# Kernel optimization log

Measured on AMD Instinct MI355X. Metric: run time of the kernel, lower is better.

## Reference

```python
import jax, jax.numpy as jnp
import numpy as np

D = 1024      # hidden_dim
V = 8         # op_vocab_size / num_ops
L = 4         # prog_len
CD = 8        # concept_dim_total (6 + 2)
I = D + CD    # op/program-generator input dim
B, T = 8, 512


def gru(x, h0, W_ih, W_hh, b_ih, b_hh):
    """PyTorch-convention GRU. x: (B,T,In), h0: (B,H). Gate order r,z,n."""
    def step(h, xt):
        gx = xt @ W_ih.T + b_ih            # (B, 3H)
        gh = h @ W_hh.T + b_hh             # (B, 3H)
        xr, xz, xn = jnp.split(gx, 3, axis=-1)
        hr, hz, hn = jnp.split(gh, 3, axis=-1)
        r = jax.nn.sigmoid(xr + hr)
        z = jax.nn.sigmoid(xz + hz)
        n = jnp.tanh(xn + r * hn)
        h_new = (1.0 - z) * n + z * h
        return h_new, h_new
    _, ys = jax.lax.scan(step, h0, jnp.swapaxes(x, 0, 1))
    return jnp.swapaxes(ys, 0, 1)          # (B,T,H)


def _l2norm(x, axis=-1):
    n = jnp.sqrt(jnp.sum(x * x, axis=axis, keepdims=True))
    return x / jnp.maximum(n, 1e-12)


def setup_inputs() -> dict:
    key = jax.random.key(0)
    ks = jax.random.split(key, 24)
    s = 0.02
    inp = {
        "x": jax.random.normal(ks[0], (B, T, D), dtype=jnp.float32),
        "attention_mask": jnp.ones((B, T), dtype=jnp.float32),
        # TemporalEncoder GRU
        "enc_Wih": s * jax.random.normal(ks[1], (3 * D, D), dtype=jnp.float32),
        "enc_Whh": s * jax.random.normal(ks[2], (3 * D, D), dtype=jnp.float32),
        "enc_bih": jnp.zeros((3 * D,), dtype=jnp.float32),
        "enc_bhh": jnp.zeros((3 * D,), dtype=jnp.float32),
        # ConceptClassifier heads (token_type=6, polarity=2)
        "tt_W": s * jax.random.normal(ks[3], (6, D), dtype=jnp.float32),
        "tt_b": jnp.zeros((6,), dtype=jnp.float32),
        "pol_W": s * jax.random.normal(ks[4], (2, D), dtype=jnp.float32),
        "pol_b": jnp.zeros((2,), dtype=jnp.float32),
        # ProgramGenerator
        "c2h_W": s * jax.random.normal(ks[5], (D, I), dtype=jnp.float32),
        "c2h_b": jnp.zeros((D,), dtype=jnp.float32),
        "pg_Wih": s * jax.random.normal(ks[6], (3 * D, I), dtype=jnp.float32),
        "pg_Whh": s * jax.random.normal(ks[7], (3 * D, D), dtype=jnp.float32),
        "pg_bih": jnp.zeros((3 * D,), dtype=jnp.float32),
        "pg_bhh": jnp.zeros((3 * D,), dtype=jnp.float32),
        "proj_W": s * jax.random.normal(ks[8], (V, D), dtype=jnp.float32),
        "proj_b": jnp.zeros((V,), dtype=jnp.float32),
        # NeuralOpLibrary: V ops, each Linear(I,D)-GELU-Linear(D,D)
        "op_W1": s * jax.random.normal(ks[9], (V, D, I), dtype=jnp.float32),
        "op_b1": jnp.zeros((V, D), dtype=jnp.float32),
        "op_W2": s * jax.random.normal(ks[10], (V, D, D), dtype=jnp.float32),
        "op_b2": jnp.zeros((V, D), dtype=jnp.float32),
        # output projection (2D -> D)
        "out_W": s * jax.random.normal(ks[11], (D, 2 * D), dtype=jnp.float32),
        "out_b": jnp.zeros((D,), dtype=jnp.float32),
    }
    return inp


def reference(x, attention_mask, enc_Wih, enc_Whh, enc_bih, enc_bhh,
              tt_W, tt_b, pol_W, pol_b, c2h_W, c2h_b,
              pg_Wih, pg_Whh, pg_bih, pg_bhh, proj_W, proj_b,
              op_W1, op_b1, op_W2, op_b2, out_W, out_b):
    Bx = x.shape[0]
    x = x * attention_mask[..., None]
    # TemporalEncoder: GRU + residual
    h0 = jnp.zeros((Bx, D), dtype=x.dtype)
    x = gru(x, h0, enc_Wih, enc_Whh, enc_bih, enc_bhh) + x        # (B,T,D)

    # concepts
    tt = x @ tt_W.T + tt_b                                        # (B,T,6)
    pol = x @ pol_W.T + pol_b                                     # (B,T,2)
    concept_summary = jnp.concatenate([tt.mean(1), pol.mean(1)], axis=-1)  # (B,8)
    pooled = x.mean(1)                                            # (B,D)
    context = jnp.concatenate([pooled, concept_summary], axis=-1) # (B,I)

    # ProgramGenerator: GRU over zero inputs, h0 from context
    pg_h0 = context @ c2h_W.T + c2h_b                             # (B,D)
    rnn_in = jnp.zeros((Bx, L, I), dtype=x.dtype)
    rnn_out = gru(rnn_in, pg_h0, pg_Wih, pg_Whh, pg_bih, pg_bhh)  # (B,L,D)
    program_logits = rnn_out @ proj_W.T + proj_b                  # (B,L,V)

    # NeuralOpLibrary. The torch code expands token feats to (B,L,T,D) and runs
    # each op redundantly per L; since op outputs are independent of L, the
    # softmax-weighted sum + mean over L equals weighting by the L-averaged
    # softmax weights (identical math).
    token_feats = jnp.concatenate([x, tt, pol], axis=-1)          # (B,T,I)
    h1 = jax.nn.gelu(jnp.einsum('bti,vdi->btvd', token_feats, op_W1) + op_b1,
                     approximate=False)                           # (B,T,V,D)
    op_out = jnp.einsum('btvh,vdh->btvd', h1, op_W2) + op_b2      # (B,T,V,D)
    w = jax.nn.softmax(program_logits, axis=-1).mean(axis=1)      # (B,V)
    out = jnp.einsum('btvd,bv->btd', op_out, w)                   # (B,T,D)

    max_pooled = out.max(axis=1)
    mean_pooled = out.mean(axis=1)
    pooled2 = jnp.concatenate([max_pooled, mean_pooled], axis=-1) # (B,2D)
    z = pooled2 @ out_W.T + out_b                                 # (B,D)

    plf = program_logits.reshape(Bx, -1)                          # (B,L*V)
    pooled_norm = _l2norm(pooled2)
    sim = pooled_norm @ pooled_norm.T                             # (B,B)
    sq = jnp.sum(plf * plf, axis=-1)
    d2 = jnp.maximum(sq[:, None] + sq[None, :] - 2.0 * (plf @ plf.T), 0.0)
    dist = jnp.where(d2 > 0, jnp.sqrt(jnp.where(d2 > 0, d2, 1.0)), 0.0)
    reuse_loss = (sim * dist).mean()

    prog_norm = _l2norm(plf)
    prog_sim = prog_norm @ prog_norm.T
    pos_mask = (sim > 0.7).astype(x.dtype)
    neg_mask = (sim < 0.7).astype(x.dtype)
    pos_loss = (1.0 - prog_sim) * pos_mask
    neg_loss = jax.nn.relu(prog_sim - 0.5) * neg_mask
    contrastive_loss = (pos_loss.sum() + neg_loss.sum()) / (pos_mask.sum() + neg_mask.sum() + 1e-6)
    return (z, reuse_loss, contrastive_loss)
```

## Files before the change

kernel.cpp:

```cpp
#include <hip/hip_runtime.h>
#include <stdint.h>

#define D_   1024
#define T_   512
#define B_   8
#define V_   8
#define I_   1032
#define KP_  1088
#define TDK  3072

typedef __attribute__((ext_vector_type(8))) short bf16x8;
typedef __attribute__((ext_vector_type(4))) float f32x4;

__device__ __forceinline__ ushort f2bf(float f){
  union{ unsigned u; float f; } c; c.f = f;
  unsigned u = c.u;
  return (ushort)((u + 0x7FFFu + ((u>>16)&1u)) >> 16);
}
__device__ __forceinline__ float bf2f(ushort h){
  union{ unsigned u; float f; } c; c.u = ((unsigned)h) << 16; return c.f;
}
__device__ __forceinline__ float sigmoidf_(float x){ return 1.f/(1.f+__expf(-x)); }

#define WAITV(N) do{ asm volatile("s_waitcnt vmcnt(" #N ")" ::: "memory"); __builtin_amdgcn_sched_barrier(0); }while(0)

__device__ __forceinline__ void gload_lds16(const void* g, void* l){
  __builtin_amdgcn_global_load_lds((const __attribute__((address_space(1))) void*)g,
                                   (__attribute__((address_space(3))) void*)l, 16, 0, 0);
}

__global__ __launch_bounds__(256) void k_prep(const float* __restrict__ x, const float* __restrict__ mask,
                                              float* __restrict__ xm, ushort* __restrict__ xmb){
  int i = blockIdx.x*256 + threadIdx.x;
  float4 v = ((const float4*)x)[i];
  float mk = mask[i >> 8];
  v.x*=mk; v.y*=mk; v.z*=mk; v.w*=mk;
  ((float4*)xm)[i] = v;
  ushort4 h; h.x=f2bf(v.x); h.y=f2bf(v.y); h.z=f2bf(v.z); h.w=f2bf(v.w);
  ((ushort4*)xmb)[i] = h;
}

__global__ __launch_bounds__(256) void k_hinit(unsigned* __restrict__ hw){
  hw[blockIdx.x*256 + threadIdx.x] = 1u;
}

__global__ __launch_bounds__(256) void k_cvt(const float* __restrict__ in, ushort* __restrict__ out, int n4){
  int i = blockIdx.x*256 + threadIdx.x;
  if (i < n4){
    float4 v = ((const float4*)in)[i];
    ushort4 h; h.x=f2bf(v.x); h.y=f2bf(v.y); h.z=f2bf(v.z); h.w=f2bf(v.w);
    ((ushort4*)out)[i] = h;
  }
}

__global__ __launch_bounds__(256) void k_cvt_w1(const float* __restrict__ w1, ushort* __restrict__ w1b){
  int row = blockIdx.x;
  const float* src = w1 + (size_t)row*I_;
  ushort* dst = w1b + (size_t)row*KP_;
  for (int c = threadIdx.x; c < KP_; c += 256){
    float v = (c < I_) ? src[c] : 0.f;
    dst[c] = f2bf(v);
  }
}

__global__ __launch_bounds__(256) void k_cvt_w2t(const float* __restrict__ w2, ushort* __restrict__ w2t){
  int blk = blockIdx.x;
  int v = blk >> 10, d = blk & 1023;
  const float4* src = (const float4*)(w2 + ((size_t)(v*1024 + d))*1024);
  ushort* dst = w2t + (size_t)d*8192 + v*1024;
  int i = threadIdx.x;
  float4 u = src[i];
  ushort4 h; h.x=f2bf(u.x); h.y=f2bf(u.y); h.z=f2bf(u.z); h.w=f2bf(u.w);
  ((ushort4*)dst)[i] = h;
}

struct EpiArgs {
  float* outf; ushort* outh;
  const float* bias; const float* wvp; const float* obias;
  int ldc;
};

template<int EPI, bool INIT>
__global__ __launch_bounds__(256) void k_gemm(const ushort* __restrict__ A, const ushort* __restrict__ Bm,
                                              int lda, int ldb, int K, EpiArgs e)
{
  __shared__ ushort As[128*64];
  __shared__ ushort Bs[128*64];
  const int tid = threadIdx.x;
  const int w = tid >> 6, l = tid & 63;
  const int wr = w >> 1, wc = w & 1;
  f32x4 acc[4][4] = {};
  const size_t arow = (size_t)(blockIdx.x*128);
  const size_t brow = (size_t)(blockIdx.y*128);
  const int lr = l >> 3, lcol = (l & 7) << 3;

  for (int k0 = 0; k0 < K; k0 += 64){
    __syncthreads();
    #pragma unroll
    for (int g = 0; g < 4; ++g){
      const int chunk = (g<<2) + w;
      const int row = (chunk<<3) + lr;
      gload_lds16(A + (arow + row)*lda + k0 + lcol, &As[chunk<<9]);
      gload_lds16(Bm + (brow + row)*ldb + k0 + lcol, &Bs[chunk<<9]);
    }
    __syncthreads();
    #pragma unroll
    for (int kk = 0; kk < 2; ++kk){
      bf16x8 af[4], bfr[4];
      #pragma unroll
      for (int m=0;m<4;++m) af[m]  = *(const bf16x8*)&As[(wr*64 + m*16 + (l&15))*64 + kk*32 + ((l>>4)<<3)];
      #pragma unroll
      for (int n=0;n<4;++n) bfr[n] = *(const bf16x8*)&Bs[(wc*64 + n*16 + (l&15))*64 + kk*32 + ((l>>4)<<3)];
      #pragma unroll
      for (int m=0;m<4;++m)
        #pragma unroll
        for (int n=0;n<4;++n)
          acc[m][n] = __builtin_amdgcn_mfma_f32_16x16x32_bf16(af[m], bfr[n], acc[m][n], 0, 0, 0);
    }
  }
  const int row0 = blockIdx.x*128 + wr*64 + ((l>>4)<<2);
  const int col0 = blockIdx.y*128 + wc*64 + (l&15);
  #pragma unroll
  for (int m=0;m<4;++m){
    #pragma unroll
    for (int n=0;n<4;++n){
      f32x4 a = acc[m][n];
      int col = col0 + n*16;
      #pragma unroll
      for (int q=0;q<4;++q){
        int row = row0 + m*16 + q;
        float val = a[q];
        if constexpr (EPI==0){
          e.outf[(size_t)row*e.ldc + col] = val + e.bias[col];
        } else if constexpr (EPI==1){
          float xg = val + e.bias[col];
          float g = 0.5f*xg*(1.0f + erff(xg*0.70710678118f));
          e.outh[(size_t)row*e.ldc + col] = f2bf(g * e.wvp[(row>>9)*V_ + (col>>10)]);
        } else {
          size_t idx = (size_t)row*e.ldc + col;
          float prev = INIT ? e.obias[((row>>9)<<10) + col] : e.outf[idx];
          e.outf[idx] = prev + val;
        }
      }
    }
  }
}

__global__ __launch_bounds__(256, 1) void k_gru4(const float* __restrict__ whh, const float* __restrict__ bhh,
                                                 const float* __restrict__ gx, unsigned* __restrict__ hw)
{
  __shared__ ushort Hld[4][8][264];
  __shared__ float Red[2][1536];
  const int tid = threadIdx.x, c = blockIdx.x;
  const int w = tid >> 6, l = tid & 63;
  const int ar = l & 15, kg = (l >> 4) << 3;

  bf16x8 Bf[3][8];
  #pragma unroll
  for (int g = 0; g < 3; ++g){
    #pragma unroll
    for (int s = 0; s < 8; ++s){
      const float* src = whh + ((size_t)((g<<10) + (c<<4) + ar))*1024 + (w<<8) + (s<<5) + kg;
      float4 u0 = *(const float4*)src;
      float4 u1 = *(const float4*)(src + 4);
      bf16x8 f;
      f[0]=(short)f2bf(u0.x); f[1]=(short)f2bf(u0.y); f[2]=(short)f2bf(u0.z); f[3]=(short)f2bf(u0.w);
      f[4]=(short)f2bf(u1.x); f[5]=(short)f2bf(u1.y); f[6]=(short)f2bf(u1.z); f[7]=(short)f2bf(u1.w);
      Bf[g][s] = f;
    }
  }
  const int pb = (w << 1) + ((l >> 4) & 1);
  const int pi = l & 15;
  const int dg = (c << 4) + pi;
  const float bhr = bhh[dg], bhz = bhh[1024 + dg], bhn = bhh[2048 + dg];
  float hp = 0.f;
  __syncthreads();

  for (int t = 0; t < 512; ++t){
    float xr, xz, xn;
    if (l < 32){
      const float* g0 = gx + ((size_t)(pb*512 + t))*TDK + dg;
      asm volatile("global_load_dword %0, %1, off" : "=v"(xr) : "v"(g0)        : "memory");
      asm volatile("global_load_dword %0, %1, off" : "=v"(xz) : "v"(g0 + 1024) : "memory");
      asm volatile("global_load_dword %0, %1, off" : "=v"(xn) : "v"(g0 + 2048) : "memory");
    }
    uint4 rw[8];
    unsigned ok = 0;
    const unsigned tagv = (unsigned)(t + 1);
    const unsigned* qb = hw + ((size_t)t << 13) + (w << 8) + (l << 2);
    while (true){
      #pragma unroll
      for (int j = 0; j < 8; ++j){
        if (!(ok & (1u << j))){
          asm volatile("global_load_dwordx4 %0, %1, off sc0 sc1" : "=v"(rw[j]) : "v"(qb + (j << 10)) : "memory");
        }
      }
      WAITV(0);
      #pragma unroll
      for (int j = 0; j < 8; ++j){
        if (!(ok & (1u << j))){
          unsigned m = (rw[j].x ^ tagv) | (rw[j].y ^ tagv) | (rw[j].z ^ tagv) | (rw[j].w ^ tagv);
          if ((m & 0xFFFFu) == 0u) ok |= (1u << j);
        }
      }
      if (__all(ok == 0xFFu)) break;
    }
    #pragma unroll
    for (int j = 0; j < 8; ++j){
      unsigned d0 = __builtin_amdgcn_perm(rw[j].y, rw[j].x, 0x07060302u);
      unsigned d1 = __builtin_amdgcn_perm(rw[j].w, rw[j].z, 0x07060302u);
      union { unsigned u[2]; unsigned long long ull; } cv; cv.u[0]=d0; cv.u[1]=d1;
      *(unsigned long long*)&Hld[w][j][l<<2] = cv.ull;
    }
    f32x4 ac0 = {0.f,0.f,0.f,0.f}, ac1 = {0.f,0.f,0.f,0.f}, ac2 = {0.f,0.f,0.f,0.f};
    #pragma unroll
    for (int s = 0; s < 8; ++s){
      bf16x8 af = *(const bf16x8*)&Hld[w][ar & 7][(s << 5) + kg];
      ac0 = __builtin_amdgcn_mfma_f32_16x16x32_bf16(af, Bf[0][s], ac0, 0, 0, 0);
      ac1 = __builtin_amdgcn_mfma_f32_16x16x32_bf16(af, Bf[1][s], ac1, 0, 0, 0);
      ac2 = __builtin_amdgcn_mfma_f32_16x16x32_bf16(af, Bf[2][s], ac2, 0, 0, 0);
    }
    const int cur = t & 1;
    if (l < 32){
      *(f32x4*)(&Red[cur][(w*3+0)*128 + l*4]) = ac0;
      *(f32x4*)(&Red[cur][(w*3+1)*128 + l*4]) = ac1;
      *(f32x4*)(&Red[cur][(w*3+2)*128 + l*4]) = ac2;
    }
    __syncthreads();
    if (l < 32){
      const int idx = (((pb>>2)<<4) | pi)*4 + (pb & 3);
      const float* R = Red[cur];
      float ghr = R[idx]       + R[384 + idx]  + R[768 + idx]  + R[1152 + idx];
      float ghz = R[128 + idx] + R[512 + idx]  + R[896 + idx]  + R[1280 + idx];
      float ghn = R[256 + idx] + R[640 + idx]  + R[1024 + idx] + R[1408 + idx];
      float r  = sigmoidf_(xr + ghr + bhr);
      float z  = sigmoidf_(xz + ghz + bhz);
      float nn = tanhf(xn + r*(ghn + bhn));
      hp = (1.f - z)*nn + z*hp;
      unsigned word = (((unsigned)f2bf(hp)) << 16) | (unsigned)(t + 2);
      unsigned* hdst = hw + ((size_t)(t+1) << 13) + (pb << 10) + dg;
      asm volatile("global_store_dword %0, %1, off sc0 sc1" :: "v"(hdst), "v"(word) : "memory");
    }
  }
}

__global__ __launch_bounds__(256) void k_tokfeat(const unsigned* __restrict__ hw, const float* __restrict__ xm,
                                                 const float* __restrict__ ttW, const float* __restrict__ ttb,
                                                 const float* __restrict__ polW, const float* __restrict__ polb,
                                                 ushort* __restrict__ tf, float* __restrict__ ttpol){
  __shared__ float xe[1024];
  const int tok = blockIdx.x;
  const int b = tok >> 9, t = tok & 511;
  const int tid = threadIdx.x;
  uint4 hv4 = *((const uint4*)(hw + ((size_t)(t+1) << 13) + ((size_t)b << 10)) + tid);
  float4 xv = ((const float4*)(xm + (size_t)tok*1024))[tid];
  float4 ev;
  ev.x = bf2f((ushort)(hv4.x >> 16)) + xv.x;
  ev.y = bf2f((ushort)(hv4.y >> 16)) + xv.y;
  ev.z = bf2f((ushort)(hv4.z >> 16)) + xv.z;
  ev.w = bf2f((ushort)(hv4.w >> 16)) + xv.w;
  *(float4*)&xe[tid*4] = ev;
  ushort4 eb; eb.x=f2bf(ev.x); eb.y=f2bf(ev.y); eb.z=f2bf(ev.z); eb.w=f2bf(ev.w);
  *(ushort4*)&tf[(size_t)tok*KP_ + tid*4] = eb;
  __syncthreads();
  const int j = tid >> 5, ln = tid & 31;
  const float* Wr = (j < 6) ? (ttW + j*1024) : (polW + (j-6)*1024);
  float acc = 0.f;
  for (int k = ln; k < 1024; k += 32) acc += xe[k]*Wr[k];
  #pragma unroll
  for (int m=16; m>=1; m>>=1) acc += __shfl_xor(acc, m, 32);
  if (ln == 0){
    float val = acc + ((j<6)? ttb[j] : polb[j-6]);
    ttpol[(size_t)tok*8 + j] = val;
    tf[(size_t)tok*KP_ + 1024 + j] = f2bf(val);
  }
  if (tid < 56) tf[(size_t)tok*KP_ + 1032 + tid] = 0;
}

__global__ __launch_bounds__(128) void k_pooled(const unsigned* __restrict__ hw, const float* __restrict__ xm,
                                                float* __restrict__ pooled){
  const int b = blockIdx.x >> 3;
  const int d = ((blockIdx.x & 7) << 7) + threadIdx.x;
  float s = 0.f;
  for (int t=0; t<512; ++t)
    s += bf2f((ushort)(hw[((size_t)(t+1) << 13) + (b << 10) + d] >> 16)) + xm[((size_t)(b*512+t)<<10) + d];
  pooled[(b<<10)+d] = s * (1.f/512.f);
}

__global__ __launch_bounds__(64) void k_csum(const float* __restrict__ ttpol, float* __restrict__ csum){
  const int b = threadIdx.x >> 3, j = threadIdx.x & 7;
  float s = 0.f;
  for (int t=0; t<512; ++t) s += ttpol[((size_t)(b*512+t)<<3) + j];
  csum[threadIdx.x] = s * (1.f/512.f);
}

__global__ __launch_bounds__(256) void k_ctx(const float* __restrict__ pooled, const float* __restrict__ csum,
                                             const float* __restrict__ c2hW, const float* __restrict__ c2hb,
                                             float* __restrict__ pgh0){
  const int i = blockIdx.x*256 + threadIdx.x;
  const int b = i >> 10, d = i & 1023;
  const float* wr = c2hW + (size_t)d*I_;
  const float* pb = pooled + (b<<10);
  float acc = c2hb[d];
  for (int k=0; k<1024; ++k) acc += pb[k]*wr[k];
  #pragma unroll
  for (int k=0; k<8; ++k) acc += csum[b*8+k]*wr[1024+k];
  pgh0[i] = acc;
}

__global__ __launch_bounds__(256) void k_pg(const float* __restrict__ whh, const float* __restrict__ bih,
                                            const float* __restrict__ bhh, const float* __restrict__ hin,
                                            float* __restrict__ hout){
  __shared__ float sh[8][1024];
  const int tid = threadIdx.x;
  for (int f = tid; f < 2048; f += 256) ((float4*)&sh[0][0])[f] = ((const float4*)hin)[f];
  __syncthreads();
  const int d = blockIdx.x*8 + (tid>>5), ln = tid & 31;
  const float* wr = whh + (size_t)d*1024;
  const float* wz = whh + (size_t)(1024+d)*1024;
  const float* wn = whh + (size_t)(2048+d)*1024;
  float ar[8]={0,0,0,0,0,0,0,0}, az[8]={0,0,0,0,0,0,0,0}, an[8]={0,0,0,0,0,0,0,0};
  for (int k = ln; k < 1024; k += 32){
    float r_=wr[k], z_=wz[k], n_=wn[k];
    #pragma unroll
    for (int b=0;b<8;++b){ float h = sh[b][k]; ar[b]+=h*r_; az[b]+=h*z_; an[b]+=h*n_; }
  }
  #pragma unroll
  for (int m=16; m>=1; m>>=1){
    #pragma unroll
    for (int b=0;b<8;++b){ ar[b]+=__shfl_xor(ar[b],m,32); az[b]+=__shfl_xor(az[b],m,32); an[b]+=__shfl_xor(an[b],m,32); }
  }
  if (ln == 0){
    float xr=bih[d], xz=bih[1024+d], xn=bih[2048+d];
    float br=bhh[d], bz=bhh[1024+d], bn=bhh[2048+d];
    #pragma unroll
    for (int b=0;b<8;++b){
      float r = sigmoidf_(xr + ar[b] + br);
      float z = sigmoidf_(xz + az[b] + bz);
      float nn = tanhf(xn + r*(an[b] + bn));
      hout[(b<<10)+d] = (1.f - z)*nn + z*sh[b][d];
    }
  }
}

__global__ __launch_bounds__(256) void k_wlogits(const float* __restrict__ pgh, const float* __restrict__ prjW,
                                                 const float* __restrict__ prjb, float* __restrict__ plog,
                                                 float* __restrict__ wv){
  __shared__ float lg[256];
  __shared__ float sm[256];
  const int tid = threadIdx.x;
  const int b = tid>>5, li = (tid>>3)&3, v = tid&7;
  const float* h = pgh + (size_t)(li+1)*8192 + (b<<10);
  const float* pw = prjW + (v<<10);
  float acc = prjb[v];
  for (int k=0;k<1024;++k) acc += h[k]*pw[k];
  lg[tid] = acc;
  plog[tid] = acc;
  __syncthreads();
  if (tid < 32){
    const int bb = tid>>2, ll = tid&3;
    const float* row = &lg[bb*32 + ll*8];
    float mx = row[0];
    #pragma unroll
    for (int u=1;u<8;++u) mx = fmaxf(mx, row[u]);
    float e[8], s=0.f;
    #pragma unroll
    for (int u=0;u<8;++u){ e[u]=__expf(row[u]-mx); s+=e[u]; }
    #pragma unroll
    for (int u=0;u<8;++u) sm[(bb*4+ll)*8+u] = e[u]/s;
  }
  __syncthreads();
  if (tid < 64){
    const int bb = tid>>3, u = tid&7;
    float s = sm[(bb*4+0)*8+u] + sm[(bb*4+1)*8+u] + sm[(bb*4+2)*8+u] + sm[(bb*4+3)*8+u];
    wv[bb*8+u] = 0.25f*s;
  }
}

__global__ __launch_bounds__(256) void k_obias(const float* __restrict__ wv, const float* __restrict__ opb2,
                                               float* __restrict__ obias){
  const int i = blockIdx.x*256 + threadIdx.x;
  const int b = i>>10, d = i&1023;
  float s = 0.f;
  #pragma unroll
  for (int v=0; v<8; ++v) s += wv[b*8+v]*opb2[(v<<10)+d];
  obias[i] = s;
}

__global__ __launch_bounds__(128) void k_pool2(const float* __restrict__ outb, float* __restrict__ pooled2){
  const int b = blockIdx.x >> 3;
  const int col = ((blockIdx.x & 7) << 7) + threadIdx.x;
  float mx = -3.4e38f, sm = 0.f;
  for (int t=0; t<512; ++t){
    float v = outb[((size_t)(b*512+t)<<10) + col];
    mx = fmaxf(mx, v); sm += v;
  }
  pooled2[((size_t)b<<11) + col] = mx;
  pooled2[((size_t)b<<11) + 1024 + col] = sm*(1.f/512.f);
}

__global__ __launch_bounds__(256) void k_z(const float* __restrict__ pooled2, const float* __restrict__ outW,
                                           const float* __restrict__ outBias, float* __restrict__ dout){
  __shared__ float p2[2048];
  const int o = blockIdx.x << 3;
  const int b = o >> 10, dbase = o & 1023;
  for (int f = threadIdx.x; f < 512; f += 256)
    ((float4*)p2)[f] = ((const float4*)(pooled2 + ((size_t)b<<11)))[f];
  __syncthreads();
  const int g = threadIdx.x >> 5, ln = threadIdx.x & 31;
  const int d = dbase + g;
  const float* wr = outW + ((size_t)d << 11);
  float acc = 0.f;
  for (int k = ln; k < 2048; k += 32) acc += p2[k]*wr[k];
  #pragma unroll
  for (int m=16; m>=1; m>>=1) acc += __shfl_xor(acc, m, 32);
  if (ln == 0) dout[(b<<10) + d] = acc + outBias[d];
}

__global__ __launch_bounds__(64) void k_losses(const float* __restrict__ p2g, const float* __restrict__ plog,
                                               float* __restrict__ dout){
  __shared__ float p2n[8], sq[8], pn[8];
  const int l = threadIdx.x;
  { const int b=l>>3, p=l&7; float s=0.f;
    const float* row = p2g + ((size_t)b<<11) + (p<<8);
    for (int k=0;k<256;++k){ float v=row[k]; s += v*v; }
    s += __shfl_xor(s,4,8); s += __shfl_xor(s,2,8); s += __shfl_xor(s,1,8);
    if (p==0) p2n[b] = fmaxf(sqrtf(s), 1e-12f);
  }
  if (l < 8){
    float s=0.f;
    #pragma unroll
    for (int k=0;k<32;++k){ float v=plog[l*32+k]; s+=v*v; }
    sq[l]=s; pn[l]=fmaxf(sqrtf(s),1e-12f);
  }
  __syncthreads();
  const int i=l>>3, j=l&7;
  const float* ri = p2g + ((size_t)i<<11);
  const float* rj = p2g + ((size_t)j<<11);
  float dot=0.f; for (int k=0;k<2048;++k) dot += ri[k]*rj[k];
  float sim = dot/(p2n[i]*p2n[j]);
  float pd=0.f;
  #pragma unroll
  for (int k=0;k<32;++k) pd += plog[i*32+k]*plog[j*32+k];
  float d2 = fmaxf(sq[i]+sq[j]-2.f*pd, 0.f);
  float dist = (d2>0.f)? sqrtf(d2) : 0.f;
  float psim = pd/(pn[i]*pn[j]);
  float pos = (sim>0.7f)?1.f:0.f, neg = (sim<0.7f)?1.f:0.f;
  float rs = sim*dist, ps=(1.f-psim)*pos, ns=fmaxf(psim-0.5f,0.f)*neg, pc=pos, nc=neg;
  #pragma unroll
  for (int m=32; m>=1; m>>=1){
    rs+=__shfl_xor(rs,m); ps+=__shfl_xor(ps,m); ns+=__shfl_xor(ns,m);
    pc+=__shfl_xor(pc,m); nc+=__shfl_xor(nc,m);
  }
  if (l==0){ dout[8192]=rs*(1.f/64.f); dout[8193]=(ps+ns)/(pc+nc+1e-6f); }
}

extern "C" void kernel_launch(void* const* d_in, const int* in_sizes, int n_in,
                              void* d_out, int out_size, void* d_ws, size_t ws_size,
                              hipStream_t stream) {
  (void)in_sizes; (void)n_in; (void)out_size; (void)ws_size;
  const float* x     = (const float*)d_in[0];
  const float* amask = (const float*)d_in[1];
  const float* eWih  = (const float*)d_in[2];
  const float* eWhh  = (const float*)d_in[3];
  const float* ebih  = (const float*)d_in[4];
  const float* ebhh  = (const float*)d_in[5];
  const float* ttW   = (const float*)d_in[6];
  const float* ttb   = (const float*)d_in[7];
  const float* polW  = (const float*)d_in[8];
  const float* polb  = (const float*)d_in[9];
  const float* c2hW  = (const float*)d_in[10];
  const float* c2hb  = (const float*)d_in[11];
  const float* pgWhh = (const float*)d_in[13];
  const float* pgbih = (const float*)d_in[14];
  const float* pgbhh = (const float*)d_in[15];
  const float* prjW  = (const float*)d_in[16];
  const float* prjb  = (const float*)d_in[17];
  const float* opW1  = (const float*)d_in[18];
  const float* opb1  = (const float*)d_in[19];
  const float* opW2  = (const float*)d_in[20];
  const float* opb2  = (const float*)d_in[21];
  const float* outW  = (const float*)d_in[22];
  const float* outB  = (const float*)d_in[23];
  float* dout = (float*)d_out;

  char* ws = (char*)d_ws;
  size_t off = 0;
  auto alloc = [&](size_t bytes)->void*{ void* p = ws + off; off += (bytes + 255) & ~(size_t)255; return p; };
  char*     R       = (char*)   alloc(64ULL*1024*1024);
  float*    xm      = (float*)  R;
  float*    gx      = (float*) (R + 16ULL*1024*1024);
  ushort*   h1g     = (ushort*) R;
  ushort*   xmb     = (ushort*)  alloc(4096ULL*1024*2);
  ushort*   wihb    = (ushort*)  alloc(3072ULL*1024*2);
  unsigned* hw      = (unsigned*)alloc(513ULL*8192*4);
  float*    ttpol   = (float*)   alloc(4096ULL*8*4);
  ushort*   tf      = (ushort*)  alloc(4096ULL*KP_*2);
  ushort*   w1b     = (ushort*)  alloc(8ULL*1024*KP_*2);
  ushort*   w2t     = (ushort*)  alloc(1024ULL*8192*2);
  float*    outbuf  = (float*)   alloc(4096ULL*1024*4);
  float*    pooled  = (float*)   alloc(8192*4);
  float*    csum    = (float*)   alloc(64*4);
  float*    pgh     = (float*)   alloc(5ULL*8192*4);
  float*    plog    = (float*)   alloc(256*4);
  float*    wv      = (float*)   alloc(64*4);
  float*    obias   = (float*)   alloc(8192*4);
  float*    pooled2 = (float*)   alloc(16384*4);

  k_hinit<<<32, 256, 0, stream>>>(hw);
  k_prep<<<4096, 256, 0, stream>>>(x, amask, xm, xmb);
  k_cvt<<<3072, 256, 0, stream>>>(eWih, wihb, 3072*1024/4);
  k_cvt_w1<<<8192, 256, 0, stream>>>(opW1, w1b);
  k_cvt_w2t<<<8192, 256, 0, stream>>>(opW2, w2t);

  { EpiArgs e{}; e.outf = gx; e.bias = ebih; e.ldc = TDK;
    k_gemm<0,false><<<dim3(32,24), 256, 0, stream>>>(xmb, wihb, 1024, 1024, 1024, e); }

  k_gru4<<<64, 256, 0, stream>>>(eWhh, ebhh, gx, hw);

  k_tokfeat<<<4096, 256, 0, stream>>>(hw, xm, ttW, ttb, polW, polb, tf, ttpol);
  k_pooled<<<64, 128, 0, stream>>>(hw, xm, pooled);
  k_csum<<<1, 64, 0, stream>>>(ttpol, csum);

  k_ctx<<<32, 256, 0, stream>>>(pooled, csum, c2hW, c2hb, pgh);
  for (int t = 0; t < 4; ++t)
    k_pg<<<128, 256, 0, stream>>>(pgWhh, pgbih, pgbhh, pgh + (size_t)t*8192, pgh + (size_t)(t+1)*8192);
  k_wlogits<<<1, 256, 0, stream>>>(pgh, prjW, prjb, plog, wv);
  k_obias<<<32, 256, 0, stream>>>(wv, opb2, obias);

  { EpiArgs e{}; e.outh = h1g; e.bias = opb1; e.wvp = wv; e.ldc = 8192;
    k_gemm<1,false><<<dim3(32,64), 256, 0, stream>>>(tf, w1b, KP_, KP_, KP_, e); }
  { EpiArgs e{}; e.outf = outbuf; e.obias = obias; e.ldc = 1024;
    k_gemm<2,true><<<dim3(32,8), 256, 0, stream>>>(h1g, w2t, 8192, 8192, 8192, e); }

  k_pool2<<<64, 128, 0, stream>>>(outbuf, pooled2);
  k_z<<<1024, 256, 0, stream>>>(pooled2, outW, outB, dout);
  k_losses<<<1, 64, 0, stream>>>(pooled2, plog, dout);
}
```

Measured before the change: 1.689 ms.

## Fuse input GEMM, GRU recurrence, weight conversion and token features into persistent megakernel

Launches one persistent kernel in which 64 blocks run the GRU recurrence while 192 helper blocks compute the input-gate GEMM in time-quarter chunks, signalling completion through global flags. The helpers also convert the op weights and compute token features as the GRU watermark advances. The separate pooled kernel is replaced by in-GRU hidden-state sums plus a helper-computed x sum. The goal is to hide the GEMM, conversion and feature work behind the latency-bound serial recurrence, at the cost of spin-wait synchronisation and possible contention with the GRU blocks.

Measured after the change: 1.620 ms. -4.1%, faster.

```diff
diff --git a/kernel.cpp b/kernel.cpp
--- a/kernel.cpp
+++ b/kernel.cpp
@@ -8,6 +8,8 @@
 #define I_   1032
 #define KP_  1088
 #define TDK  3072
+#define NGRU 64
+#define NHELP 192
 
 typedef __attribute__((ext_vector_type(8))) short bf16x8;
 typedef __attribute__((ext_vector_type(4))) float f32x4;
@@ -22,7 +24,8 @@
 }
 __device__ __forceinline__ float sigmoidf_(float x){ return 1.f/(1.f+__expf(-x)); }
 
-#define WAITV(N) do{ asm volatile("s_waitcnt vmcnt(" #N ")" ::: "memory"); __builtin_amdgcn_sched_barrier(0); }while(0)
+#define WAITV0 do{ asm volatile("s_waitcnt vmcnt(0)" ::: "memory"); __builtin_amdgcn_sched_barrier(0); }while(0)
+#define WAITV3 do{ asm volatile("s_waitcnt vmcnt(3)" ::: "memory"); __builtin_amdgcn_sched_barrier(0); }while(0)
 
 __device__ __forceinline__ void gload_lds16(const void* g, void* l){
   __builtin_amdgcn_global_load_lds((const __attribute__((address_space(1))) void*)g,
@@ -51,27 +54,6 @@
     ushort4 h; h.x=f2bf(v.x); h.y=f2bf(v.y); h.z=f2bf(v.z); h.w=f2bf(v.w);
     ((ushort4*)out)[i] = h;
   }
-}
-
-__global__ __launch_bounds__(256) void k_cvt_w1(const float* __restrict__ w1, ushort* __restrict__ w1b){
-  int row = blockIdx.x;
-  const float* src = w1 + (size_t)row*I_;
-  ushort* dst = w1b + (size_t)row*KP_;
-  for (int c = threadIdx.x; c < KP_; c += 256){
-    float v = (c < I_) ? src[c] : 0.f;
-    dst[c] = f2bf(v);
-  }
-}
-
-__global__ __launch_bounds__(256) void k_cvt_w2t(const float* __restrict__ w2, ushort* __restrict__ w2t){
-  int blk = blockIdx.x;
-  int v = blk >> 10, d = blk & 1023;
-  const float4* src = (const float4*)(w2 + ((size_t)(v*1024 + d))*1024);
-  ushort* dst = w2t + (size_t)d*8192 + v*1024;
-  int i = threadIdx.x;
-  float4 u = src[i];
-  ushort4 h; h.x=f2bf(u.x); h.y=f2bf(u.y); h.z=f2bf(u.z); h.w=f2bf(u.w);
-  ((ushort4*)dst)[i] = h;
 }
 
 struct EpiArgs {
@@ -130,9 +112,7 @@
       for (int q=0;q<4;++q){
         int row = row0 + m*16 + q;
         float val = a[q];
-        if constexpr (EPI==0){
-          e.outf[(size_t)row*e.ldc + col] = val + e.bias[col];
-        } else if constexpr (EPI==1){
+        if constexpr (EPI==1){
           float xg = val + e.bias[col];
           float g = 0.5f*xg*(1.0f + erff(xg*0.70710678118f));
           e.outh[(size_t)row*e.ldc + col] = f2bf(g * e.wvp[(row>>9)*V_ + (col>>10)]);
@@ -146,145 +126,312 @@
   }
 }
 
-__global__ __launch_bounds__(256, 1) void k_gru4(const float* __restrict__ whh, const float* __restrict__ bhh,
-                                                 const float* __restrict__ gx, unsigned* __restrict__ hw)
+__global__ __launch_bounds__(256, 1) void k_mega(
+    const float* __restrict__ whh, const float* __restrict__ bhh,
+    const ushort* __restrict__ xmb, const ushort* __restrict__ wihb,
+    const float* __restrict__ ebih, float* __restrict__ gx,
+    unsigned* __restrict__ hw, const float* __restrict__ xm,
+    const float* __restrict__ ttW, const float* __restrict__ ttb,
+    const float* __restrict__ polW, const float* __restrict__ polb,
+    ushort* __restrict__ tf, float* __restrict__ ttpol,
+    const float* __restrict__ opW1, ushort* __restrict__ w1b,
+    const float* __restrict__ opW2, ushort* __restrict__ w2t,
+    float* __restrict__ hsum, float* __restrict__ xsum,
+    int* __restrict__ done, int* __restrict__ wm)
 {
-  __shared__ ushort Hld[4][8][264];
-  __shared__ float Red[2][1536];
-  const int tid = threadIdx.x, c = blockIdx.x;
+  __shared__ char smem[32768];
+  const int tid = threadIdx.x;
   const int w = tid >> 6, l = tid & 63;
-  const int ar = l & 15, kg = (l >> 4) << 3;
-
-  bf16x8 Bf[3][8];
-  #pragma unroll
-  for (int g = 0; g < 3; ++g){
-    #pragma unroll
-    for (int s = 0; s < 8; ++s){
-      const float* src = whh + ((size_t)((g<<10) + (c<<4) + ar))*1024 + (w<<8) + (s<<5) + kg;
-      float4 u0 = *(const float4*)src;
-      float4 u1 = *(const float4*)(src + 4);
-      bf16x8 f;
-      f[0]=(short)f2bf(u0.x); f[1]=(short)f2bf(u0.y); f[2]=(short)f2bf(u0.z); f[3]=(short)f2bf(u0.w);
-      f[4]=(short)f2bf(u1.x); f[5]=(short)f2bf(u1.y); f[6]=(short)f2bf(u1.z); f[7]=(short)f2bf(u1.w);
-      Bf[g][s] = f;
-    }
-  }
-  const int pb = (w << 1) + ((l >> 4) & 1);
-  const int pi = l & 15;
-  const int dg = (c << 4) + pi;
-  const float bhr = bhh[dg], bhz = bhh[1024 + dg], bhn = bhh[2048 + dg];
-  float hp = 0.f;
-  __syncthreads();
-
-  for (int t = 0; t < 512; ++t){
-    float xr, xz, xn;
+
+  if (blockIdx.x < NGRU){
+    const int c = blockIdx.x;
+    const int ar = l & 15, kg = (l >> 4) << 3;
+    ushort (*Hld)[264] = (ushort (*)[264])smem;
+    float* Red = (float*)(smem + 4*8*264*2);
+
+    bf16x8 Bf[3][8];
+    #pragma unroll
+    for (int g = 0; g < 3; ++g){
+      #pragma unroll
+      for (int s = 0; s < 8; ++s){
+        const float* src = whh + ((size_t)((g<<10) + (c<<4) + ar))*1024 + (w<<8) + (s<<5) + kg;
+        float4 u0 = *(const float4*)src;
+        float4 u1 = *(const float4*)(src + 4);
+        bf16x8 f;
+        f[0]=(short)f2bf(u0.x); f[1]=(short)f2bf(u0.y); f[2]=(short)f2bf(u0.z); f[3]=(short)f2bf(u0.w);
+        f[4]=(short)f2bf(u1.x); f[5]=(short)f2bf(u1.y); f[6]=(short)f2bf(u1.z); f[7]=(short)f2bf(u1.w);
+        Bf[g][s] = f;
+      }
+    }
+    const int pb = (w << 1) + ((l >> 4) & 1);
+    const int pi = l & 15;
+    const int dg = (c << 4) + pi;
+    const float bhr = bhh[dg], bhz = bhh[1024 + dg], bhn = bhh[2048 + dg];
+    float hp = 0.f, hacc = 0.f;
+    __syncthreads();
+
+    {
+      const int* dp = done + l*3;
+      int f0, f1, f2;
+      while (true){
+        asm volatile("global_load_dword %0, %1, off sc0 sc1" : "=v"(f0) : "v"(dp)   : "memory");
+        asm volatile("global_load_dword %0, %1, off sc0 sc1" : "=v"(f1) : "v"(dp+1) : "memory");
+        asm volatile("global_load_dword %0, %1, off sc0 sc1" : "=v"(f2) : "v"(dp+2) : "memory");
+        WAITV0;
+        if (__all((f0 & f1 & f2) == 1)) break;
+        __builtin_amdgcn_s_sleep(4);
+      }
+    }
+    __syncthreads();
+    float xr, xz, xn, nxr, nxz, nxn;
     if (l < 32){
-      const float* g0 = gx + ((size_t)(pb*512 + t))*TDK + dg;
-      asm volatile("global_load_dword %0, %1, off" : "=v"(xr) : "v"(g0)        : "memory");
-      asm volatile("global_load_dword %0, %1, off" : "=v"(xz) : "v"(g0 + 1024) : "memory");
-      asm volatile("global_load_dword %0, %1, off" : "=v"(xn) : "v"(g0 + 2048) : "memory");
-    }
-    uint4 rw[8];
-    unsigned ok = 0;
-    const unsigned tagv = (unsigned)(t + 1);
-    const unsigned* qb = hw + ((size_t)t << 13) + (w << 8) + (l << 2);
-    while (true){
+      const float* g0 = gx + ((size_t)(pb*512))*TDK + dg;
+      asm volatile("global_load_dword %0, %1, off sc0 sc1" : "=v"(xr) : "v"(g0)        : "memory");
+      asm volatile("global_load_dword %0, %1, off sc0 sc1" : "=v"(xz) : "v"(g0 + 1024) : "memory");
+      asm volatile("global_load_dword %0, %1, off sc0 sc1" : "=v"(xn) : "v"(g0 + 2048) : "memory");
+    }
+    WAITV0;
+
+    for (int t = 0; t < 512; ++t){
+      if ((t & 127) == 0 && t){
+        const int tq = t >> 7;
+        const int* dp = done + tq*192 + l*3;
+        int f0, f1, f2;
+        while (true){
+          asm volatile("global_load_dword %0, %1, off sc0 sc1" : "=v"(f0) : "v"(dp)   : "memory");
+          asm volatile("global_load_dword %0, %1, off sc0 sc1" : "=v"(f1) : "v"(dp+1) : "memory");
+          asm volatile("global_load_dword %0, %1, off sc0 sc1" : "=v"(f2) : "v"(dp+2) : "memory");
+          WAITV0;
+          if (__all((f0 & f1 & f2) == 1)) break;
+          __builtin_amdgcn_s_sleep(4);
+        }
+        __syncthreads();
+        if (l < 32){
+          const float* g0 = gx + ((size_t)(pb*512 + t))*TDK + dg;
+          asm volatile("global_load_dword %0, %1, off sc0 sc1" : "=v"(xr) : "v"(g0)        : "memory");
+          asm volatile("global_load_dword %0, %1, off sc0 sc1" : "=v"(xz) : "v"(g0 + 1024) : "memory");
+          asm volatile("global_load_dword %0, %1, off sc0 sc1" : "=v"(xn) : "v"(g0 + 2048) : "memory");
+        }
+        WAITV0;
+      }
+      uint4 rw[8];
+      unsigned ok = 0;
+      const unsigned tagv = (unsigned)(t + 1);
+      const unsigned* qb = hw + ((size_t)t << 13) + (w << 8) + (l << 2);
+      #pragma unroll
+      for (int j = 0; j < 8; ++j)
+        asm volatile("global_load_dwordx4 %0, %1, off sc0 sc1" : "=v"(rw[j]) : "v"(qb + (j << 10)) : "memory");
+      const bool gxi = (((t+1) & 127) != 0) && (t+1 < 512);
+      if (gxi && l < 32){
+        const float* g0 = gx + ((size_t)(pb*512 + t + 1))*TDK + dg;
+        asm volatile("global_load_dword %0, %1, off sc0 sc1" : "=v"(nxr) : "v"(g0)        : "memory");
+        asm volatile("global_load_dword %0, %1, off sc0 sc1" : "=v"(nxz) : "v"(g0 + 1024) : "memory");
+        asm volatile("global_load_dword %0, %1, off sc0 sc1" : "=v"(nxn) : "v"(g0 + 2048) : "memory");
+      }
+      if (gxi) { WAITV3; } else { WAITV0; }
       #pragma unroll
       for (int j = 0; j < 8; ++j){
-        if (!(ok & (1u << j))){
-          asm volatile("global_load_dwordx4 %0, %1, off sc0 sc1" : "=v"(rw[j]) : "v"(qb + (j << 10)) : "memory");
-        }
-      }
-      WAITV(0);
+        unsigned m = (rw[j].x ^ tagv) | (rw[j].y ^ tagv) | (rw[j].z ^ tagv) | (rw[j].w ^ tagv);
+        if ((m & 0xFFFFu) == 0u) ok |= (1u << j);
+      }
+      while (!__all(ok == 0xFFu)){
+        #pragma unroll
+        for (int j = 0; j < 8; ++j){
+          if (!(ok & (1u << j)))
+            asm volatile("global_load_dwordx4 %0, %1, off sc0 sc1" : "=v"(rw[j]) : "v"(qb + (j << 10)) : "memory");
+        }
+        WAITV0;
+        #pragma unroll
+        for (int j = 0; j < 8; ++j){
+          if (!(ok & (1u << j))){
+            unsigned m = (rw[j].x ^ tagv) | (rw[j].y ^ tagv) | (rw[j].z ^ tagv) | (rw[j].w ^ tagv);
+            if ((m & 0xFFFFu) == 0u) ok |= (1u << j);
+          }
+        }
+      }
       #pragma unroll
       for (int j = 0; j < 8; ++j){
-        if (!(ok & (1u << j))){
-          unsigned m = (rw[j].x ^ tagv) | (rw[j].y ^ tagv) | (rw[j].z ^ tagv) | (rw[j].w ^ tagv);
-          if ((m & 0xFFFFu) == 0u) ok |= (1u << j);
-        }
-      }
-      if (__all(ok == 0xFFu)) break;
-    }
-    #pragma unroll
-    for (int j = 0; j < 8; ++j){
-      unsigned d0 = __builtin_amdgcn_perm(rw[j].y, rw[j].x, 0x07060302u);
-      unsigned d1 = __builtin_amdgcn_perm(rw[j].w, rw[j].z, 0x07060302u);
-      union { unsigned u[2]; unsigned long long ull; } cv; cv.u[0]=d0; cv.u[1]=d1;
-      *(unsigned long long*)&Hld[w][j][l<<2] = cv.ull;
-    }
-    f32x4 ac0 = {0.f,0.f,0.f,0.f}, ac1 = {0.f,0.f,0.f,0.f}, ac2 = {0.f,0.f,0.f,0.f};
-    #pragma unroll
-    for (int s = 0; s < 8; ++s){
-      bf16x8 af = *(const bf16x8*)&Hld[w][ar & 7][(s << 5) + kg];
-      ac0 = __builtin_amdgcn_mfma_f32_16x16x32_bf16(af, Bf[0][s], ac0, 0, 0, 0);
-      ac1 = __builtin_amdgcn_mfma_f32_16x16x32_bf16(af, Bf[1][s], ac1, 0, 0, 0);
-      ac2 = __builtin_amdgcn_mfma_f32_16x16x32_bf16(af, Bf[2][s], ac2, 0, 0, 0);
-    }
-    const int cur = t & 1;
-    if (l < 32){
-      *(f32x4*)(&Red[cur][(w*3+0)*128 + l*4]) = ac0;
-      *(f32x4*)(&Red[cur][(w*3+1)*128 + l*4]) = ac1;
-      *(f32x4*)(&Red[cur][(w*3+2)*128 + l*4]) = ac2;
-    }
-    __syncthreads();
-    if (l < 32){
-      const int idx = (((pb>>2)<<4) | pi)*4 + (pb & 3);
-      const float* R = Red[cur];
-      float ghr = R[idx]       + R[384 + idx]  + R[768 + idx]  + R[1152 + idx];
-      float ghz = R[128 + idx] + R[512 + idx]  + R[896 + idx]  + R[1280 + idx];
-      float ghn = R[256 + idx] + R[640 + idx]  + R[1024 + idx] + R[1408 + idx];
-      float r  = sigmoidf_(xr + ghr + bhr);
-      float z  = sigmoidf_(xz + ghz + bhz);
-      float nn = tanhf(xn + r*(ghn + bhn));
-      hp = (1.f - z)*nn + z*hp;
-      unsigned word = (((unsigned)f2bf(hp)) << 16) | (unsigned)(t + 2);
-      unsigned* hdst = hw + ((size_t)(t+1) << 13) + (pb << 10) + dg;
-      asm volatile("global_store_dword %0, %1, off sc0 sc1" :: "v"(hdst), "v"(word) : "memory");
-    }
-  }
-}
-
-__global__ __launch_bounds__(256) void k_tokfeat(const unsigned* __restrict__ hw, const float* __restrict__ xm,
-                                                 const float* __restrict__ ttW, const float* __restrict__ ttb,
-                                                 const float* __restrict__ polW, const float* __restrict__ polb,
-                                                 ushort* __restrict__ tf, float* __restrict__ ttpol){
-  __shared__ float xe[1024];
-  const int tok = blockIdx.x;
-  const int b = tok >> 9, t = tok & 511;
-  const int tid = threadIdx.x;
-  uint4 hv4 = *((const uint4*)(hw + ((size_t)(t+1) << 13) + ((size_t)b << 10)) + tid);
-  float4 xv = ((const float4*)(xm + (size_t)tok*1024))[tid];
-  float4 ev;
-  ev.x = bf2f((ushort)(hv4.x >> 16)) + xv.x;
-  ev.y = bf2f((ushort)(hv4.y >> 16)) + xv.y;
-  ev.z = bf2f((ushort)(hv4.z >> 16)) + xv.z;
-  ev.w = bf2f((ushort)(hv4.w >> 16)) + xv.w;
-  *(float4*)&xe[tid*4] = ev;
-  ushort4 eb; eb.x=f2bf(ev.x); eb.y=f2bf(ev.y); eb.z=f2bf(ev.z); eb.w=f2bf(ev.w);
-  *(ushort4*)&tf[(size_t)tok*KP_ + tid*4] = eb;
-  __syncthreads();
-  const int j = tid >> 5, ln = tid & 31;
-  const float* Wr = (j < 6) ? (ttW + j*1024) : (polW + (j-6)*1024);
-  float acc = 0.f;
-  for (int k = ln; k < 1024; k += 32) acc += xe[k]*Wr[k];
-  #pragma unroll
-  for (int m=16; m>=1; m>>=1) acc += __shfl_xor(acc, m, 32);
-  if (ln == 0){
-    float val = acc + ((j<6)? ttb[j] : polb[j-6]);
-    ttpol[(size_t)tok*8 + j] = val;
-    tf[(size_t)tok*KP_ + 1024 + j] = f2bf(val);
-  }
-  if (tid < 56) tf[(size_t)tok*KP_ + 1032 + tid] = 0;
-}
-
-__global__ __launch_bounds__(128) void k_pooled(const unsigned* __restrict__ hw, const float* __restrict__ xm,
-                                                float* __restrict__ pooled){
-  const int b = blockIdx.x >> 3;
-  const int d = ((blockIdx.x & 7) << 7) + threadIdx.x;
-  float s = 0.f;
-  for (int t=0; t<512; ++t)
-    s += bf2f((ushort)(hw[((size_t)(t+1) << 13) + (b << 10) + d] >> 16)) + xm[((size_t)(b*512+t)<<10) + d];
-  pooled[(b<<10)+d] = s * (1.f/512.f);
+        unsigned d0 = __builtin_amdgcn_perm(rw[j].y, rw[j].x, 0x07060302u);
+        unsigned d1 = __builtin_amdgcn_perm(rw[j].w, rw[j].z, 0x07060302u);
+        union { unsigned u[2]; unsigned long long ull; } cv; cv.u[0]=d0; cv.u[1]=d1;
+        *(unsigned long long*)&Hld[w*8 + j][l<<2] = cv.ull;
+      }
+      f32x4 ac0 = {0.f,0.f,0.f,0.f}, ac1 = {0.f,0.f,0.f,0.f}, ac2 = {0.f,0.f,0.f,0.f};
+      #pragma unroll
+      for (int s = 0; s < 8; ++s){
+        bf16x8 af = *(const bf16x8*)&Hld[w*8 + (ar & 7)][(s << 5) + kg];
+        ac0 = __builtin_amdgcn_mfma_f32_16x16x32_bf16(af, Bf[0][s], ac0, 0, 0, 0);
+        ac1 = __builtin_amdgcn_mfma_f32_16x16x32_bf16(af, Bf[1][s], ac1, 0, 0, 0);
+        ac2 = __builtin_amdgcn_mfma_f32_16x16x32_bf16(af, Bf[2][s], ac2, 0, 0, 0);
+      }
+      const int cur = t & 1;
+      if (l < 32){
+        *(f32x4*)(&Red[cur*1536 + (w*3+0)*128 + l*4]) = ac0;
+        *(f32x4*)(&Red[cur*1536 + (w*3+1)*128 + l*4]) = ac1;
+        *(f32x4*)(&Red[cur*1536 + (w*3+2)*128 + l*4]) = ac2;
+      }
+      __syncthreads();
+      if (l < 32){
+        const int idx = (((pb>>2)<<4) | pi)*4 + (pb & 3);
+        const float* R = Red + cur*1536;
+        float ghr = R[idx]       + R[384 + idx]  + R[768 + idx]  + R[1152 + idx];
+        float ghz = R[128 + idx] + R[512 + idx]  + R[896 + idx]  + R[1280 + idx];
+        float ghn = R[256 + idx] + R[640 + idx]  + R[1024 + idx] + R[1408 + idx];
+        float r  = sigmoidf_(xr + ghr + bhr);
+        float z  = sigmoidf_(xz + ghz + bhz);
+        float nn = tanhf(xn + r*(ghn + bhn));
+        hp = (1.f - z)*nn + z*hp;
+        hacc += hp;
+        unsigned word = (((unsigned)f2bf(hp)) << 16) | (unsigned)(t + 2);
+        unsigned* hdst = hw + ((size_t)(t+1) << 13) + (pb << 10) + dg;
+        asm volatile("global_store_dword %0, %1, off sc0 sc1" :: "v"(hdst), "v"(word) : "memory");
+      }
+      if (c == 0 && tid == 0){
+        asm volatile("global_store_dword %0, %1, off sc0 sc1" :: "v"(wm), "v"(t) : "memory");
+      }
+      if (gxi && l < 32){ xr = nxr; xz = nxz; xn = nxn; }
+    }
+    if (l < 32) hsum[(pb << 10) + dg] = hacc;
+    return;
+  }
+
+  const int hid = blockIdx.x - NGRU;
+  ushort* As = (ushort*)smem;
+  ushort* Bs = As + 8192;
+
+  {
+    const int bb = hid / 24, ni = hid % 24;
+    const int wr_ = w >> 1, wc_ = w & 1;
+    const int lr = l >> 3, lcol = (l & 7) << 3;
+    for (int wv = 0; wv < 4; ++wv){
+      const int mi = bb*4 + wv;
+      f32x4 acc[4][4] = {};
+      for (int k0 = 0; k0 < 1024; k0 += 64){
+        __syncthreads();
+        #pragma unroll
+        for (int g = 0; g < 4; ++g){
+          const int chunk = (g<<2) + w;
+          const int row = (chunk<<3) + lr;
+          gload_lds16(xmb + (size_t)(mi*128 + row)*1024 + k0 + lcol, &As[chunk<<9]);
+          gload_lds16(wihb + (size_t)(ni*128 + row)*1024 + k0 + lcol, &Bs[chunk<<9]);
+        }
+        __syncthreads();
+        #pragma unroll
+        for (int kk = 0; kk < 2; ++kk){
+          bf16x8 af[4], bfr[4];
+          #pragma unroll
+          for (int m=0;m<4;++m) af[m]  = *(const bf16x8*)&As[(wr_*64 + m*16 + (l&15))*64 + kk*32 + ((l>>4)<<3)];
+          #pragma unroll
+          for (int n=0;n<4;++n) bfr[n] = *(const bf16x8*)&Bs[(wc_*64 + n*16 + (l&15))*64 + kk*32 + ((l>>4)<<3)];
+          #pragma unroll
+          for (int m=0;m<4;++m)
+            #pragma unroll
+            for (int n=0;n<4;++n)
+              acc[m][n] = __builtin_amdgcn_mfma_f32_16x16x32_bf16(af[m], bfr[n], acc[m][n], 0, 0, 0);
+        }
+      }
+      const int row0 = mi*128 + wr_*64 + ((l>>4)<<2);
+      const int col0 = ni*128 + wc_*64 + (l&15);
+      #pragma unroll
+      for (int m=0;m<4;++m){
+        #pragma unroll
+        for (int n=0;n<4;++n){
+          f32x4 a = acc[m][n];
+          int col = col0 + n*16;
+          float bi = ebih[col];
+          #pragma unroll
+          for (int q=0;q<4;++q){
+            int row = row0 + m*16 + q;
+            float val = a[q] + bi;
+            float* p = gx + (size_t)row*TDK + col;
+            asm volatile("global_store_dword %0, %1, off sc0 sc1" :: "v"(p), "v"(val) : "memory");
+          }
+        }
+      }
+      WAITV0;
+      __syncthreads();
+      if (tid == 0){
+        int one = 1;
+        const int* fp = done + wv*192 + hid;
+        asm volatile("global_store_dword %0, %1, off sc0 sc1" :: "v"(fp), "v"(one) : "memory");
+      }
+      __syncthreads();
+    }
+  }
+  for (int row = hid; row < 8192; row += NHELP){
+    const float* src = opW1 + (size_t)row*I_;
+    ushort* dst = w1b + (size_t)row*KP_;
+    for (int cc = tid; cc < KP_; cc += 256){
+      float v = (cc < I_) ? src[cc] : 0.f;
+      dst[cc] = f2bf(v);
+    }
+  }
+  for (int blk = hid; blk < 8192; blk += NHELP){
+    const int v = blk >> 10, d = blk & 1023;
+    const float4* src = (const float4*)(opW2 + ((size_t)(v*1024 + d))*1024);
+    ushort* dst = w2t + (size_t)d*8192 + v*1024;
+    float4 u = src[tid];
+    ushort4 h; h.x=f2bf(u.x); h.y=f2bf(u.y); h.z=f2bf(u.z); h.w=f2bf(u.w);
+    ((ushort4*)dst)[tid] = h;
+  }
+  if (hid < 32){
+    const int o = hid*256 + tid;
+    const int b = o >> 10, d = o & 1023;
+    float s = 0.f;
+    for (int t = 0; t < 512; ++t) s += xm[((size_t)(b*512 + t) << 10) + d];
+    xsum[o] = s;
+  }
+  {
+    float* xe = (float*)smem;
+    for (int idx = hid; idx < 4096; idx += NHELP){
+      const int t = idx >> 3, b = idx & 7;
+      const int tok = b*512 + t;
+      const int need = (t+1 < 511) ? (t+1) : 511;
+      if (tid == 0){
+        int wmv;
+        while (true){
+          asm volatile("global_load_dword %0, %1, off sc0 sc1" : "=v"(wmv) : "v"(wm) : "memory");
+          asm volatile("s_waitcnt vmcnt(0)" ::: "memory");
+          if (wmv >= need) break;
+          __builtin_amdgcn_s_sleep(64);
+        }
+      }
+      __syncthreads();
+      const unsigned tagv = (unsigned)(t + 2);
+      const unsigned* src = hw + ((size_t)(t+1) << 13) + (b << 10) + (tid << 2);
+      uint4 hv;
+      while (true){
+        asm volatile("global_load_dwordx4 %0, %1, off sc0 sc1" : "=v"(hv) : "v"(src) : "memory");
+        WAITV0;
+        unsigned m = (hv.x ^ tagv) | (hv.y ^ tagv) | (hv.z ^ tagv) | (hv.w ^ tagv);
+        if (__syncthreads_and((int)((m & 0xFFFFu) == 0u))) break;
+        __builtin_amdgcn_s_sleep(16);
+      }
+      float4 xv = ((const float4*)(xm + (size_t)tok*1024))[tid];
+      float4 ev;
+      ev.x = bf2f((ushort)(hv.x >> 16)) + xv.x;
+      ev.y = bf2f((ushort)(hv.y >> 16)) + xv.y;
+      ev.z = bf2f((ushort)(hv.z >> 16)) + xv.z;
+      ev.w = bf2f((ushort)(hv.w >> 16)) + xv.w;
+      *(float4*)&xe[tid*4] = ev;
+      ushort4 eb; eb.x=f2bf(ev.x); eb.y=f2bf(ev.y); eb.z=f2bf(ev.z); eb.w=f2bf(ev.w);
+      *(ushort4*)&tf[(size_t)tok*KP_ + tid*4] = eb;
+      __syncthreads();
+      const int j = tid >> 5, ln = tid & 31;
+      const float* Wr = (j < 6) ? (ttW + j*1024) : (polW + (j-6)*1024);
+      float acc = 0.f;
+      for (int k = ln; k < 1024; k += 32) acc += xe[k]*Wr[k];
+      #pragma unroll
+      for (int m=16; m>=1; m>>=1) acc += __shfl_xor(acc, m, 32);
+      if (ln == 0){
+        float val = acc + ((j<6)? ttb[j] : polb[j-6]);
+        ttpol[(size_t)tok*8 + j] = val;
+        tf[(size_t)tok*KP_ + 1024 + j] = f2bf(val);
+      }
+      if (tid < 56) tf[(size_t)tok*KP_ + 1032 + tid] = 0;
+      __syncthreads();
+    }
+  }
 }
 
 __global__ __launch_bounds__(64) void k_csum(const float* __restrict__ ttpol, float* __restrict__ csum){
@@ -294,15 +441,18 @@
   csum[threadIdx.x] = s * (1.f/512.f);
 }
 
-__global__ __launch_bounds__(256) void k_ctx(const float* __restrict__ pooled, const float* __restrict__ csum,
+__global__ __launch_bounds__(256) void k_ctx(const float* __restrict__ hsum, const float* __restrict__ xsum,
+                                             const float* __restrict__ csum,
                                              const float* __restrict__ c2hW, const float* __restrict__ c2hb,
                                              float* __restrict__ pgh0){
   const int i = blockIdx.x*256 + threadIdx.x;
   const int b = i >> 10, d = i & 1023;
   const float* wr = c2hW + (size_t)d*I_;
-  const float* pb = pooled + (b<<10);
-  float acc = c2hb[d];
-  for (int k=0; k<1024; ++k) acc += pb[k]*wr[k];
+  const float* hs = hsum + (b<<10);
+  const float* xs = xsum + (b<<10);
+  float s = 0.f;
+  for (int k=0; k<1024; ++k) s += (hs[k]+xs[k])*wr[k];
+  float acc = c2hb[d] + s*(1.f/512.f);
   #pragma unroll
   for (int k=0; k<8; ++k) acc += csum[b*8+k]*wr[1024+k];
   pgh0[i] = acc;
@@ -499,30 +649,30 @@
   ushort*   w1b     = (ushort*)  alloc(8ULL*1024*KP_*2);
   ushort*   w2t     = (ushort*)  alloc(1024ULL*8192*2);
   float*    outbuf  = (float*)   alloc(4096ULL*1024*4);
-  float*    pooled  = (float*)   alloc(8192*4);
+  float*    hsum    = (float*)   alloc(8192*4);
+  float*    xsum    = (float*)   alloc(8192*4);
   float*    csum    = (float*)   alloc(64*4);
   float*    pgh     = (float*)   alloc(5ULL*8192*4);
   float*    plog    = (float*)   alloc(256*4);
   float*    wv      = (float*)   alloc(64*4);
   float*    obias   = (float*)   alloc(8192*4);
   float*    pooled2 = (float*)   alloc(16384*4);
-
+  int*      ctrl    = (int*)     alloc(4096);
+  int*      done    = ctrl;
+  int*      wm      = ctrl + 896;
+
+  hipMemsetAsync(done, 0, 4*192*4, stream);
+  hipMemsetAsync(wm, 0xFF, 4, stream);
   k_hinit<<<32, 256, 0, stream>>>(hw);
   k_prep<<<4096, 256, 0, stream>>>(x, amask, xm, xmb);
   k_cvt<<<3072, 256, 0, stream>>>(eWih, wihb, 3072*1024/4);
-  k_cvt_w1<<<8192, 256, 0, stream>>>(opW1, w1b);
-  k_cvt_w2t<<<8192, 256, 0, stream>>>(opW2, w2t);
-
-  { EpiArgs e{}; e.outf = gx; e.bias = ebih; e.ldc = TDK;
-    k_gemm<0,false><<<dim3(32,24), 256, 0, stream>>>(xmb, wihb, 1024, 1024, 1024, e); }
-
-  k_gru4<<<64, 256, 0, stream>>>(eWhh, ebhh, gx, hw);
-
-  k_tokfeat<<<4096, 256, 0, stream>>>(hw, xm, ttW, ttb, polW, polb, tf, ttpol);
-  k_pooled<<<64, 128, 0, stream>>>(hw, xm, pooled);
+
+  k_mega<<<256, 256, 0, stream>>>(eWhh, ebhh, xmb, wihb, ebih, gx, hw, xm,
+                                  ttW, ttb, polW, polb, tf, ttpol,
+                                  opW1, w1b, opW2, w2t, hsum, xsum, done, wm);
+
   k_csum<<<1, 64, 0, stream>>>(ttpol, csum);
-
-  k_ctx<<<32, 256, 0, stream>>>(pooled, csum, c2hW, c2hb, pgh);
+  k_ctx<<<32, 256, 0, stream>>>(hsum, xsum, csum, c2hW, c2hb, pgh);
   for (int t = 0; t < 4; ++t)
     k_pg<<<128, 256, 0, stream>>>(pgWhh, pgbih, pgbhh, pgh + (size_t)t*8192, pgh + (size_t)(t+1)*8192);
   k_wlogits<<<1, 256, 0, stream>>>(pgh, prjW, prjb, plog, wv);
```
